# Kernel tuning notes

Hardware: AMD Instinct MI355X
Metric: run time of the kernel (lower is better)

The kernel has to match this reference:

```python
import jax, jax.numpy as jnp
import numpy as np

B, C_IN, H, W = 16, 128, 224, 224
C_OUT, KH, KW = 256, 3, 3
STRIDE = (2, 3)
PAD = 1


def setup_inputs() -> dict:
    key = jax.random.key(0)
    kx, kw, kb = jax.random.split(key, 3)
    x = jax.random.normal(kx, (B, C_IN, H, W), dtype=jnp.float32)
    weight = jax.random.normal(kw, (C_OUT, C_IN, KH, KW), dtype=jnp.float32)
    bias = jax.random.normal(kb, (C_OUT,), dtype=jnp.float32)
    return {"x": x, "weight": weight, "bias": bias}


def reference(x, weight, bias):
    # Faithful conv2d: zero-pad by 1 on each side, stride (2,3), kernel 3x3,
    # per-output-channel dot product + bias (same math as the quadruple-loop torch code).
    out = jax.lax.conv_general_dilated(
        x, weight,
        window_strides=STRIDE,
        padding=[(PAD, PAD), (PAD, PAD)],
        dimension_numbers=("NCHW", "OIHW", "NCHW"),
    )
    return out + bias[None, :, None, None]
```

## Files before the change

kernel.cpp:

```cpp
#include <hip/hip_runtime.h>
#include <cstdint>

constexpr int B_   = 16;
constexpr int CIN  = 128;
constexpr int H_   = 224;
constexpr int W_   = 224;
constexpr int COUT = 256;
constexpr int HOUT = 112;
constexpr int WOUT = 75;

constexpr int OWP   = 80;
constexpr int BM    = 160;
constexpr int CI_SC = 16;
constexpr int KSC_R = 144;
constexpr int KP    = 160;
constexpr int NSC   = 8;
constexpr int THREADS = 512;

constexpr int WS_SH8  = COUT * KP * NSC / 8;
constexpr size_t WS_NEED = (size_t)WS_SH8 * 16;

typedef float  f32x4  __attribute__((ext_vector_type(4)));
typedef short  short8 __attribute__((ext_vector_type(8)));

struct U64x2 { unsigned long long lo, hi; };
__device__ inline short8 bc8(unsigned long long a, unsigned long long b) {
  U64x2 u{a, b};
  return __builtin_bit_cast(short8, u);
}

__device__ inline unsigned cvtpk(float a, float b) {
  unsigned r;
  asm("v_cvt_pk_bf16_f32 %0, %1, %2" : "=v"(r) : "v"(a), "v"(b));
  return r;
}

__global__ __launch_bounds__(256) void wprep(const float* __restrict__ wgt,
                                             uint4* __restrict__ ws) {
  int o  = blockIdx.x * 256 + threadIdx.x;
  int co = o & 255;
  int t  = o >> 8;
  int g  = t & 3;
  int u  = t >> 2;
  int kc = u % 5;
  int sc = u / 5;
  int kloc = kc * 32 + g * 8;
  float f[8];
  if (kloc < KSC_R) {
    const float* p = wgt + (size_t)co * 1152 + sc * KSC_R + kloc;
    float4 a = *(const float4*)p;
    float4 b = *(const float4*)(p + 4);
    f[0] = a.x; f[1] = a.y; f[2] = a.z; f[3] = a.w;
    f[4] = b.x; f[5] = b.y; f[6] = b.z; f[7] = b.w;
  } else {
#pragma unroll
    for (int e = 0; e < 8; ++e) f[e] = 0.f;
  }
  ws[o] = uint4{cvtpk(f[0], f[1]), cvtpk(f[2], f[3]), cvtpk(f[4], f[5]), cvtpk(f[6], f[7])};
}

__device__ __forceinline__ short8 load_bq(const float* q, int kc, int g) {
  if (kc == 4 && g >= 2) return short8{};
  const float* s = q + kc * 32;
  float4 x0 = *(const float4*)s, x1 = *(const float4*)(s + 4);
  uint4 u{cvtpk(x0.x, x0.y), cvtpk(x0.z, x0.w), cvtpk(x1.x, x1.y), cvtpk(x1.z, x1.w)};
  return __builtin_bit_cast(short8, u);
}

#define TR_ISSUE(S, KC)                                                                   \
  {                                                                                       \
    unsigned a_ = abase + (unsigned)((KC) * 10240);                                       \
    asm volatile("ds_read_b64_tr_b16 %0, %1"             : "=v"(S##0) : "v"(a_));         \
    asm volatile("ds_read_b64_tr_b16 %0, %1 offset:1280" : "=v"(S##1) : "v"(a_));         \
    asm volatile("ds_read_b64_tr_b16 %0, %1 offset:128"  : "=v"(S##2) : "v"(a_));         \
    asm volatile("ds_read_b64_tr_b16 %0, %1 offset:1408" : "=v"(S##3) : "v"(a_));         \
    asm volatile("ds_read_b64_tr_b16 %0, %1 offset:256"  : "=v"(S##4) : "v"(a_));         \
    asm volatile("ds_read_b64_tr_b16 %0, %1 offset:1536" : "=v"(S##5) : "v"(a_));         \
    asm volatile("ds_read_b64_tr_b16 %0, %1 offset:384"  : "=v"(S##6) : "v"(a_));         \
    asm volatile("ds_read_b64_tr_b16 %0, %1 offset:1664" : "=v"(S##7) : "v"(a_));         \
    asm volatile("ds_read_b64_tr_b16 %0, %1 offset:512"  : "=v"(S##8) : "v"(a_));         \
    asm volatile("ds_read_b64_tr_b16 %0, %1 offset:1792" : "=v"(S##9) : "v"(a_));         \
  }

#define BLOAD(X, KC)                                                                      \
  if (WS) {                                                                               \
    X##0 = wsb[(KC) * 1024];                                                              \
    X##1 = wsb[(KC) * 1024 + 16];                                                         \
    X##2 = wsb[(KC) * 1024 + 32];                                                         \
    X##3 = wsb[(KC) * 1024 + 48];                                                         \
  } else {                                                                                \
    X##0 = load_bq(q0, (KC), g);                                                          \
    X##1 = load_bq(q1, (KC), g);                                                          \
    X##2 = load_bq(q2, (KC), g);                                                          \
    X##3 = load_bq(q3, (KC), g);                                                          \
  }

#define WAITLG(N)                                                                         \
  asm volatile("s_waitcnt lgkmcnt(" #N ")" ::: "memory");                                 \
  __builtin_amdgcn_sched_barrier(0);

#define MFMA_SET(S, X)                                                                    \
  {                                                                                       \
    short8 a0_ = bc8(S##0, S##1);                                                         \
    short8 a1_ = bc8(S##2, S##3);                                                         \
    short8 a2_ = bc8(S##4, S##5);                                                         \
    short8 a3_ = bc8(S##6, S##7);                                                         \
    short8 a4_ = bc8(S##8, S##9);                                                         \
    __builtin_amdgcn_s_setprio(1);                                                        \
    acc[0][0] = __builtin_amdgcn_mfma_f32_16x16x32_bf16(a0_, X##0, acc[0][0], 0, 0, 0);   \
    acc[0][1] = __builtin_amdgcn_mfma_f32_16x16x32_bf16(a0_, X##1, acc[0][1], 0, 0, 0);   \
    acc[0][2] = __builtin_amdgcn_mfma_f32_16x16x32_bf16(a0_, X##2, acc[0][2], 0, 0, 0);   \
    acc[0][3] = __builtin_amdgcn_mfma_f32_16x16x32_bf16(a0_, X##3, acc[0][3], 0, 0, 0);   \
    acc[1][0] = __builtin_amdgcn_mfma_f32_16x16x32_bf16(a1_, X##0, acc[1][0], 0, 0, 0);   \
    acc[1][1] = __builtin_amdgcn_mfma_f32_16x16x32_bf16(a1_, X##1, acc[1][1], 0, 0, 0);   \
    acc[1][2] = __builtin_amdgcn_mfma_f32_16x16x32_bf16(a1_, X##2, acc[1][2], 0, 0, 0);   \
    acc[1][3] = __builtin_amdgcn_mfma_f32_16x16x32_bf16(a1_, X##3, acc[1][3], 0, 0, 0);   \
    acc[2][0] = __builtin_amdgcn_mfma_f32_16x16x32_bf16(a2_, X##0, acc[2][0], 0, 0, 0);   \
    acc[2][1] = __builtin_amdgcn_mfma_f32_16x16x32_bf16(a2_, X##1, acc[2][1], 0, 0, 0);   \
    acc[2][2] = __builtin_amdgcn_mfma_f32_16x16x32_bf16(a2_, X##2, acc[2][2], 0, 0, 0);   \
    acc[2][3] = __builtin_amdgcn_mfma_f32_16x16x32_bf16(a2_, X##3, acc[2][3], 0, 0, 0);   \
    acc[3][0] = __builtin_amdgcn_mfma_f32_16x16x32_bf16(a3_, X##0, acc[3][0], 0, 0, 0);   \
    acc[3][1] = __builtin_amdgcn_mfma_f32_16x16x32_bf16(a3_, X##1, acc[3][1], 0, 0, 0);   \
    acc[3][2] = __builtin_amdgcn_mfma_f32_16x16x32_bf16(a3_, X##2, acc[3][2], 0, 0, 0);   \
    acc[3][3] = __builtin_amdgcn_mfma_f32_16x16x32_bf16(a3_, X##3, acc[3][3], 0, 0, 0);   \
    acc[4][0] = __builtin_amdgcn_mfma_f32_16x16x32_bf16(a4_, X##0, acc[4][0], 0, 0, 0);   \
    acc[4][1] = __builtin_amdgcn_mfma_f32_16x16x32_bf16(a4_, X##1, acc[4][1], 0, 0, 0);   \
    acc[4][2] = __builtin_amdgcn_mfma_f32_16x16x32_bf16(a4_, X##2, acc[4][2], 0, 0, 0);   \
    acc[4][3] = __builtin_amdgcn_mfma_f32_16x16x32_bf16(a4_, X##3, acc[4][3], 0, 0, 0);   \
    __builtin_amdgcn_s_setprio(0);                                                        \
  }

template <int WS>
__global__ __launch_bounds__(THREADS, 2) void conv_mfma(
    const float* __restrict__ x, const float* __restrict__ wgt,
    const short8* __restrict__ wbf, const float* __restrict__ bias,
    float* __restrict__ out) {

  __shared__ __align__(16) unsigned char smem[KP * BM * 2];

  int Lid   = (blockIdx.x & 7) * 112 + (blockIdx.x >> 3);
  int ohp   = Lid % 56;
  int b     = Lid / 56;
  int oh_base = ohp * 2;

  const int tid   = threadIdx.x;
  const int lane  = tid & 63;
  const int wv    = tid >> 6;
  const int mhalf = wv >> 2;
  const int cogrp = wv & 3;
  const int g     = lane >> 4;
  const int l15   = lane & 15;

  const float* xb = x + (size_t)b * CIN * H_ * W_;
  const int coB_  = cogrp * 64 + l15;

  const unsigned sbase = (unsigned)(uintptr_t)&smem[0];
  const unsigned abase = sbase + (unsigned)(g * 2560 + mhalf * 640 + l15 * 8);

  if (tid < 320) {
    *reinterpret_cast<uint4*>(&smem[46080 + tid * 16]) = uint4{0u, 0u, 0u, 0u};
  }

  int      aoff[4], moff[4], coff[4];
  unsigned lb0[4], lb1[4], lb2[4], mA[4], mF[4];
#pragma unroll
  for (int j = 0; j < 4; ++j) {
    int it  = tid + THREADS * j;
    int gg  = it % 19;
    int rid = it / 19;
    int ci  = rid & 15;
    int t3  = rid >> 4;
    int kh  = t3 % 3;
    int ohl = t3 / 3;
    int ih  = 2 * (oh_base + ohl) - 1 + kh;
    bool rowok = (unsigned)ih < (unsigned)H_;
    int ro  = (ci * H_ + (rowok ? ih : 0)) * W_;
    int iwb = 12 * gg;
    aoff[j] = ro + iwb;
    moff[j] = ro + iwb - (gg ? 1 : 0);
    coff[j] = ro + (iwb + 8 > 220 ? 220 : iwb + 8);
    int k = ci * 9 + kh * 3;
    int m = ohl * OWP + 4 * gg;
    auto byteOf = [](int kk, int mm) -> unsigned {
      return (unsigned)(((kk >> 2) * 10 + (mm >> 4)) * 128 + (kk & 3) * 32 + (mm & 15) * 2);
    };
    lb0[j] = byteOf(k, m); lb1[j] = byteOf(k + 1, m); lb2[j] = byteOf(k + 2, m);
    mA[j] = rowok ? 0xFFFFFFFFu : 0u;
    mF[j] = mA[j] & (gg ? 0xFFFFFFFFu : 0xFFFF0000u);
  }

  f32x4 acc[5][4];
#pragma unroll
  for (int mf = 0; mf < 5; ++mf)
#pragma unroll
    for (int cf = 0; cf < 4; ++cf)
#pragma unroll
      for (int i = 0; i < 4; ++i) acc[mf][cf][i] = 0.f;

  unsigned long long tA0, tA1, tA2, tA3, tA4, tA5, tA6, tA7, tA8, tA9;
  unsigned long long tB0, tB1, tB2, tB3, tB4, tB5, tB6, tB7, tB8, tB9;
  short8 bA0, bA1, bA2, bA3, bB0, bB1, bB2, bB3;

  for (int sc = 0; sc < NSC; ++sc) {
    if (sc) __syncthreads();

    const float* xs = xb + (size_t)sc * (CI_SC * H_ * W_);
#pragma unroll
    for (int j = 0; j < 4; ++j) {
      if (j < 3 || tid < 288) {
        const float* ap = xs + aoff[j];
        float4 a4 = *(const float4*)ap;
        float4 b4 = *(const float4*)(ap + 4);
        float4 c4 = *(const float4*)(xs + coff[j]);
        float fm1 = xs[moff[j]];
        unsigned l0 = cvtpk(fm1,  a4.z) & mF[j];
        unsigned h0 = cvtpk(b4.y, c4.x) & mA[j];
        unsigned l1 = cvtpk(a4.x, a4.w) & mA[j];
        unsigned h1 = cvtpk(b4.z, c4.y) & mA[j];
        unsigned l2 = cvtpk(a4.y, b4.x) & mA[j];
        unsigned h2 = cvtpk(b4.w, c4.z) & mA[j];
        *(uint2*)&smem[lb0[j]] = make_uint2(l0, h0);
        *(uint2*)&smem[lb1[j]] = make_uint2(l1, h1);
        *(uint2*)&smem[lb2[j]] = make_uint2(l2, h2);
      }
    }
    __syncthreads();

    const short8* wsb = wbf + (size_t)sc * 5120 + g * 256 + cogrp * 64 + l15;
    const float*  q0 = wgt + (size_t)coB_ * 1152 + sc * 144 + g * 8;
    const float*  q1 = q0 + (size_t)16 * 1152;
    const float*  q2 = q0 + (size_t)32 * 1152;
    const float*  q3 = q0 + (size_t)48 * 1152;

    BLOAD(bA, 0)
    TR_ISSUE(tA, 0)
    BLOAD(bB, 1)
    TR_ISSUE(tB, 1)
    WAITLG(10)
    MFMA_SET(tA, bA)
    BLOAD(bA, 2)
    TR_ISSUE(tA, 2)
    WAITLG(10)
    MFMA_SET(tB, bB)
    BLOAD(bB, 3)
    TR_ISSUE(tB, 3)
    WAITLG(10)
    MFMA_SET(tA, bA)
    BLOAD(bA, 4)
    TR_ISSUE(tA, 4)
    WAITLG(10)
    MFMA_SET(tB, bB)
    WAITLG(0)
    MFMA_SET(tA, bA)
  }

  int oh = oh_base + mhalf;
  float bv0 = bias[coB_];
  float bv1 = bias[coB_ + 16];
  float bv2 = bias[coB_ + 32];
  float bv3 = bias[coB_ + 48];
  size_t ob0 = (((size_t)b * COUT + coB_) * HOUT + oh) * WOUT;
  size_t ob1 = ob0 + (size_t)16 * HOUT * WOUT;
  size_t ob2 = ob0 + (size_t)32 * HOUT * WOUT;
  size_t ob3 = ob0 + (size_t)48 * HOUT * WOUT;
#pragma unroll
  for (int mf = 0; mf < 5; ++mf) {
    int owb = mf * 16 + g * 4;
#pragma unroll
    for (int r = 0; r < 4; ++r) {
      int ow = owb + r;
      if (ow < WOUT) {
        out[ob0 + ow] = acc[mf][0][r] + bv0;
        out[ob1 + ow] = acc[mf][1][r] + bv1;
        out[ob2 + ow] = acc[mf][2][r] + bv2;
        out[ob3 + ow] = acc[mf][3][r] + bv3;
      }
    }
  }
}

extern "C" void kernel_launch(void* const* d_in, const int* in_sizes, int n_in,
                              void* d_out, int out_size, void* d_ws, size_t ws_size,
                              hipStream_t stream) {
  const float* x    = (const float*)d_in[0];
  const float* wgt  = (const float*)d_in[1];
  const float* bias = (const float*)d_in[2];
  float* out        = (float*)d_out;

  dim3 grid(16 * 56);
  dim3 block(THREADS);

  if (ws_size >= WS_NEED) {
    wprep<<<dim3(WS_SH8 / 256), dim3(256), 0, stream>>>(wgt, (uint4*)d_ws);
    conv_mfma<1><<<grid, block, 0, stream>>>(x, wgt, (const short8*)d_ws, bias, out);
  } else {
    conv_mfma<0><<<grid, block, 0, stream>>>(x, wgt, (const short8*)d_ws, bias, out);
  }
}
```

Baseline: 206.3 us.

## Halve block to one output row with 256 threads and raise occupancy

```diff
diff --git a/kernel.cpp b/kernel.cpp
--- a/kernel.cpp
+++ b/kernel.cpp
@@ -10,12 +10,11 @@
 constexpr int WOUT = 75;
 
 constexpr int OWP   = 80;
-constexpr int BM    = 160;
 constexpr int CI_SC = 16;
 constexpr int KSC_R = 144;
 constexpr int KP    = 160;
 constexpr int NSC   = 8;
-constexpr int THREADS = 512;
+constexpr int THREADS = 256;
 
 constexpr int WS_SH8  = COUT * KP * NSC / 8;
 constexpr size_t WS_NEED = (size_t)WS_SH8 * 16;
@@ -69,17 +68,17 @@
 
 #define TR_ISSUE(S, KC)                                                                   \
   {                                                                                       \
-    unsigned a_ = abase + (unsigned)((KC) * 10240);                                       \
+    unsigned a_ = abase + (unsigned)((KC) * 5120);                                        \
     asm volatile("ds_read_b64_tr_b16 %0, %1"             : "=v"(S##0) : "v"(a_));         \
-    asm volatile("ds_read_b64_tr_b16 %0, %1 offset:1280" : "=v"(S##1) : "v"(a_));         \
+    asm volatile("ds_read_b64_tr_b16 %0, %1 offset:640"  : "=v"(S##1) : "v"(a_));         \
     asm volatile("ds_read_b64_tr_b16 %0, %1 offset:128"  : "=v"(S##2) : "v"(a_));         \
-    asm volatile("ds_read_b64_tr_b16 %0, %1 offset:1408" : "=v"(S##3) : "v"(a_));         \
+    asm volatile("ds_read_b64_tr_b16 %0, %1 offset:768"  : "=v"(S##3) : "v"(a_));         \
     asm volatile("ds_read_b64_tr_b16 %0, %1 offset:256"  : "=v"(S##4) : "v"(a_));         \
-    asm volatile("ds_read_b64_tr_b16 %0, %1 offset:1536" : "=v"(S##5) : "v"(a_));         \
+    asm volatile("ds_read_b64_tr_b16 %0, %1 offset:896"  : "=v"(S##5) : "v"(a_));         \
     asm volatile("ds_read_b64_tr_b16 %0, %1 offset:384"  : "=v"(S##6) : "v"(a_));         \
-    asm volatile("ds_read_b64_tr_b16 %0, %1 offset:1664" : "=v"(S##7) : "v"(a_));         \
+    asm volatile("ds_read_b64_tr_b16 %0, %1 offset:1024" : "=v"(S##7) : "v"(a_));         \
     asm volatile("ds_read_b64_tr_b16 %0, %1 offset:512"  : "=v"(S##8) : "v"(a_));         \
-    asm volatile("ds_read_b64_tr_b16 %0, %1 offset:1792" : "=v"(S##9) : "v"(a_));         \
+    asm volatile("ds_read_b64_tr_b16 %0, %1 offset:1152" : "=v"(S##9) : "v"(a_));         \
   }
 
 #define BLOAD(X, KC)                                                                      \
@@ -131,23 +130,20 @@
   }
 
 template <int WS>
-__global__ __launch_bounds__(THREADS, 2) void conv_mfma(
+__global__ __launch_bounds__(THREADS, 3) void conv_mfma(
     const float* __restrict__ x, const float* __restrict__ wgt,
     const short8* __restrict__ wbf, const float* __restrict__ bias,
     float* __restrict__ out) {
 
-  __shared__ __align__(16) unsigned char smem[KP * BM * 2];
-
-  int Lid   = (blockIdx.x & 7) * 112 + (blockIdx.x >> 3);
-  int ohp   = Lid % 56;
-  int b     = Lid / 56;
-  int oh_base = ohp * 2;
+  __shared__ __align__(16) unsigned char smem[KP * OWP * 2];
+
+  int Lid = (blockIdx.x & 7) * 224 + (blockIdx.x >> 3);
+  int oh  = Lid % 112;
+  int b   = Lid / 112;
 
   const int tid   = threadIdx.x;
   const int lane  = tid & 63;
-  const int wv    = tid >> 6;
-  const int mhalf = wv >> 2;
-  const int cogrp = wv & 3;
+  const int cogrp = tid >> 6;
   const int g     = lane >> 4;
   const int l15   = lane & 15;
 
@@ -155,38 +151,10 @@
   const int coB_  = cogrp * 64 + l15;
 
   const unsigned sbase = (unsigned)(uintptr_t)&smem[0];
-  const unsigned abase = sbase + (unsigned)(g * 2560 + mhalf * 640 + l15 * 8);
-
-  if (tid < 320) {
-    *reinterpret_cast<uint4*>(&smem[46080 + tid * 16]) = uint4{0u, 0u, 0u, 0u};
-  }
-
-  int      aoff[4], moff[4], coff[4];
-  unsigned lb0[4], lb1[4], lb2[4], mA[4], mF[4];
-#pragma unroll
-  for (int j = 0; j < 4; ++j) {
-    int it  = tid + THREADS * j;
-    int gg  = it % 19;
-    int rid = it / 19;
-    int ci  = rid & 15;
-    int t3  = rid >> 4;
-    int kh  = t3 % 3;
-    int ohl = t3 / 3;
-    int ih  = 2 * (oh_base + ohl) - 1 + kh;
-    bool rowok = (unsigned)ih < (unsigned)H_;
-    int ro  = (ci * H_ + (rowok ? ih : 0)) * W_;
-    int iwb = 12 * gg;
-    aoff[j] = ro + iwb;
-    moff[j] = ro + iwb - (gg ? 1 : 0);
-    coff[j] = ro + (iwb + 8 > 220 ? 220 : iwb + 8);
-    int k = ci * 9 + kh * 3;
-    int m = ohl * OWP + 4 * gg;
-    auto byteOf = [](int kk, int mm) -> unsigned {
-      return (unsigned)(((kk >> 2) * 10 + (mm >> 4)) * 128 + (kk & 3) * 32 + (mm & 15) * 2);
-    };
-    lb0[j] = byteOf(k, m); lb1[j] = byteOf(k + 1, m); lb2[j] = byteOf(k + 2, m);
-    mA[j] = rowok ? 0xFFFFFFFFu : 0u;
-    mF[j] = mA[j] & (gg ? 0xFFFFFFFFu : 0xFFFF0000u);
+  const unsigned abase = sbase + (unsigned)(g * 1280 + l15 * 8);
+
+  if (tid < 160) {
+    *reinterpret_cast<uint4*>(&smem[23040 + tid * 16]) = uint4{0u, 0u, 0u, 0u};
   }
 
   f32x4 acc[5][4];
@@ -207,21 +175,41 @@
     const float* xs = xb + (size_t)sc * (CI_SC * H_ * W_);
 #pragma unroll
     for (int j = 0; j < 4; ++j) {
-      if (j < 3 || tid < 288) {
-        const float* ap = xs + aoff[j];
+      int it = tid + THREADS * j;
+      if (j < 3 || it < 912) {
+        int gg  = it % 19;
+        int rid = it / 19;
+        int ci  = rid & 15;
+        int kh  = rid >> 4;
+        int ih  = 2 * oh - 1 + kh;
+        bool rowok = (unsigned)ih < (unsigned)H_;
+        int ro  = (ci * H_ + (rowok ? ih : 0)) * W_;
+        int iwb = 12 * gg;
+        unsigned mAj = rowok ? 0xFFFFFFFFu : 0u;
+        unsigned mFj = mAj & (gg ? 0xFFFFFFFFu : 0xFFFF0000u);
+
+        const float* ap = xs + (ro + iwb);
         float4 a4 = *(const float4*)ap;
         float4 b4 = *(const float4*)(ap + 4);
-        float4 c4 = *(const float4*)(xs + coff[j]);
-        float fm1 = xs[moff[j]];
-        unsigned l0 = cvtpk(fm1,  a4.z) & mF[j];
-        unsigned h0 = cvtpk(b4.y, c4.x) & mA[j];
-        unsigned l1 = cvtpk(a4.x, a4.w) & mA[j];
-        unsigned h1 = cvtpk(b4.z, c4.y) & mA[j];
-        unsigned l2 = cvtpk(a4.y, b4.x) & mA[j];
-        unsigned h2 = cvtpk(b4.w, c4.z) & mA[j];
-        *(uint2*)&smem[lb0[j]] = make_uint2(l0, h0);
-        *(uint2*)&smem[lb1[j]] = make_uint2(l1, h1);
-        *(uint2*)&smem[lb2[j]] = make_uint2(l2, h2);
+        float4 c4 = *(const float4*)(xs + (ro + (iwb + 8 > 220 ? 220 : iwb + 8)));
+        float fm1 = xs[ro + iwb - (gg ? 1 : 0)];
+
+        int k = ci * 9 + kh * 3;
+        int m = 4 * gg;
+        unsigned base = (unsigned)(((k >> 2) * 5 + (m >> 4)) * 128 + (m & 15) * 2);
+        unsigned o0 = base + (unsigned)((k & 3) * 32);
+        unsigned o1 = base + (unsigned)(((k + 1) & 3) * 32) + (((k + 1) >> 2) - (k >> 2)) * 640u;
+        unsigned o2 = base + (unsigned)(((k + 2) & 3) * 32) + (((k + 2) >> 2) - (k >> 2)) * 640u;
+
+        unsigned l0 = cvtpk(fm1,  a4.z) & mFj;
+        unsigned h0 = cvtpk(b4.y, c4.x) & mAj;
+        unsigned l1 = cvtpk(a4.x, a4.w) & mAj;
+        unsigned h1 = cvtpk(b4.z, c4.y) & mAj;
+        unsigned l2 = cvtpk(a4.y, b4.x) & mAj;
+        unsigned h2 = cvtpk(b4.w, c4.z) & mAj;
+        *(uint2*)&smem[o0] = make_uint2(l0, h0);
+        *(uint2*)&smem[o1] = make_uint2(l1, h1);
+        *(uint2*)&smem[o2] = make_uint2(l2, h2);
       }
     }
     __syncthreads();
@@ -254,7 +242,6 @@
     MFMA_SET(tA, bA)
   }
 
-  int oh = oh_base + mhalf;
   float bv0 = bias[coB_];
   float bv1 = bias[coB_ + 16];
   float bv2 = bias[coB_ + 32];
@@ -287,7 +274,7 @@
   const float* bias = (const float*)d_in[2];
   float* out        = (float*)d_out;
 
-  dim3 grid(16 * 56);
+  dim3 grid(16 * 112);
   dim3 block(THREADS);
 
   if (ws_size >= WS_NEED) {
```

Result: slower. 270.6 us (+31.2%).
